# Kernel optimization log

Hardware: AMD Instinct MI355X
Metric: run time of the kernel (lower is better)

The kernel has to match this reference:

```python
import jax, jax.numpy as jnp
import numpy as np


def setup_inputs() -> dict:
    key = jax.random.key(0)
    k1, k2, k3 = jax.random.split(key, 3)
    B, A, CI, CO, E = 2048, 128, 128, 128, 4
    x = jax.random.normal(k1, (B, A, CI), dtype=jnp.float32)
    atom_numbers = jax.random.randint(k2, (B, A), 0, 9, dtype=jnp.int32)
    # glorot-uniform-ish init for W; zeros for b (matches model_ops.zeros)
    limit = np.sqrt(6.0 / (CI + CO)).astype(np.float32)
    W = jax.random.uniform(k3, (E, CI, CO), dtype=jnp.float32, minval=-limit, maxval=limit)
    b = jnp.zeros((E, CO), dtype=jnp.float32)
    atom_cases = jnp.array([1, 6, 7, 8], dtype=jnp.int32)
    return {"x": x, "atom_numbers": atom_numbers, "W": W, "b": b, "atom_cases": atom_cases}


def reference(x, atom_numbers, W, b, atom_cases):
    # Per-expert dense: h[e,b,a,o] = relu(x[b,a,:] @ W[e] + b[e])
    h = jax.nn.relu(jnp.einsum('bai,eio->ebao', x, W) + b[:, None, None, :])
    # mask[e,b,a] = 1 where atom_numbers == atom_cases[e]
    mask = (atom_numbers[None, :, :] == atom_cases[:, None, None]).astype(x.dtype)
    # masked sum over experts -> [B, max_atoms, out_channels]
    return jnp.einsum('ebao,eba->bao', h, mask)
```

## Files before the change

### kernel.cpp

```cpp
#include <hip/hip_runtime.h>
#include <hip/hip_bf16.h>
#include <stdint.h>


typedef __attribute__((ext_vector_type(8))) short short8;
typedef __attribute__((ext_vector_type(4))) float f32x4;

#define PERM_U32_OFF 65536
#define BUCKET_CAP   262144
#define OST_STRIDE   132

union U16 { uint4 u; short8 s; };

__device__ __forceinline__ int bucket_of(int v, int c0, int c1, int c2, int c3) {
    return (v == c0) ? 0 : (v == c1) ? 1 : (v == c2) ? 2 : (v == c3) ? 3 : 4;
}

__device__ __forceinline__ uint32_t pkbf(float lo, float hi) {
    __hip_bfloat162 h = __float22bfloat162_rn(make_float2(lo, hi));
    uint32_t r;
    __builtin_memcpy(&r, &h, 4);
    return r;
}

__global__ __launch_bounds__(256) void k_prep(const float* __restrict__ W,
                                              uint32_t* __restrict__ ws) {
    if (blockIdx.x == 0 && threadIdx.x < 8) ws[threadIdx.x] = 0u;
    const int T   = blockIdx.x * 256 + threadIdx.x;
    const int c16 = T & 15;
    const int g   = (T >> 4) & 3;
    const int nt  = (T >> 6) & 7;
    const int kk  = (T >> 9) & 3;
    const int e   = (T >> 11) & 3;
    float v[8];
    #pragma unroll
    for (int j = 0; j < 8; ++j)
        v[j] = W[(size_t)(e * 128 + kk * 32 + g * 8 + j) * 128 + nt * 16 + c16];
    uint4 pack = make_uint4(pkbf(v[0], v[1]), pkbf(v[2], v[3]),
                            pkbf(v[4], v[5]), pkbf(v[6], v[7]));
    const int lane = g * 16 + c16;
    *(uint4*)((char*)ws + 1024 + e * 32768 + ((kk * 8 + nt) * 64 + lane) * 16) = pack;
}

__global__ __launch_bounds__(256) void k_scatter(const int* __restrict__ an,
                                                 const int* __restrict__ cases,
                                                 uint32_t* __restrict__ ws) {
    __shared__ uint32_t lc[5], lbase[5];
    if (threadIdx.x < 5) lc[threadIdx.x] = 0u;
    __syncthreads();
    const int c0 = cases[0], c1 = cases[1], c2 = cases[2], c3 = cases[3];
    const int r0 = (blockIdx.x * 256 + threadIdx.x) * 4;
    const int4 a = *(const int4*)(an + r0);
    int bk[4];
    bk[0] = bucket_of(a.x, c0, c1, c2, c3);
    bk[1] = bucket_of(a.y, c0, c1, c2, c3);
    bk[2] = bucket_of(a.z, c0, c1, c2, c3);
    bk[3] = bucket_of(a.w, c0, c1, c2, c3);
    uint32_t slot[4];
    #pragma unroll
    for (int i = 0; i < 4; ++i) slot[i] = atomicAdd(&lc[bk[i]], 1u);
    __syncthreads();
    if (threadIdx.x < 5) lbase[threadIdx.x] = atomicAdd(&ws[threadIdx.x], lc[threadIdx.x]);
    __syncthreads();
    uint32_t* __restrict__ perm = ws + PERM_U32_OFF;
    #pragma unroll
    for (int i = 0; i < 4; ++i)
        perm[bk[i] * BUCKET_CAP + lbase[bk[i]] + slot[i]] = (uint32_t)(r0 + i);
}

__global__ __launch_bounds__(512, 4) void k_gemm(const float* __restrict__ x,
                                                 const float* __restrict__ bvec,
                                                 const uint32_t* __restrict__ ws,
                                                 float* __restrict__ out) {
    __shared__ int   ridx[128];
    __shared__ float ost[128 * OST_STRIDE];

    int b = -1, chunk = 0, accb = 0;
    #pragma unroll
    for (int bb = 0; bb < 5; ++bb) {
        const int nb = (int)((ws[bb] + 127u) >> 7);
        if (b < 0 && (int)blockIdx.x < accb + nb) { b = bb; chunk = blockIdx.x - accb; }
        accb += nb;
    }
    if (b < 0) return;

    const int cb   = (int)ws[b];
    const int rbeg = chunk << 7;
    const int nval = min(128, cb - rbeg);
    const uint32_t* __restrict__ perm = ws + PERM_U32_OFF + (size_t)b * BUCKET_CAP;
    if (threadIdx.x < 128)
        ridx[threadIdx.x] = (threadIdx.x < nval) ? (int)perm[rbeg + threadIdx.x] : -1;
    __syncthreads();

    const int lane = threadIdx.x & 63;
    const int wv   = threadIdx.x >> 6;

    if (b == 4) {
        const int half = lane >> 5, l32 = lane & 31;
        const float4 z = make_float4(0.f, 0.f, 0.f, 0.f);
        #pragma unroll
        for (int it = 0; it < 8; ++it) {
            const int r = ridx[wv * 16 + it * 2 + half];
            if (r >= 0) *(float4*)(out + (size_t)r * 128 + l32 * 4) = z;
        }
        return;
    }

    const int g4  = lane >> 4;
    const int c16 = lane & 15;
    const int rg  = wv >> 2;
    const int ng  = wv & 3;

    const float bv0 = bvec[b * 128 + (ng * 2 + 0) * 16 + c16];
    const float bv1 = bvec[b * 128 + (ng * 2 + 1) * 16 + c16];

    int arow[4];
    #pragma unroll
    for (int mf = 0; mf < 4; ++mf) arow[mf] = ridx[rg * 64 + mf * 16 + c16];

    f32x4 acc[4][2];
    #pragma unroll
    for (int mf = 0; mf < 4; ++mf) {
        acc[mf][0] = (f32x4){0.f, 0.f, 0.f, 0.f};
        acc[mf][1] = (f32x4){0.f, 0.f, 0.f, 0.f};
    }

    const uint4* __restrict__ wf = (const uint4*)((const char*)ws + 1024 + b * 32768);

    #pragma unroll
    for (int kk = 0; kk < 4; ++kk) {
        U16 wb0, wb1;
        wb0.u = wf[(kk * 8 + ng * 2 + 0) * 64 + lane];
        wb1.u = wf[(kk * 8 + ng * 2 + 1) * 64 + lane];
        short8 afr[4];
        #pragma unroll
        for (int mf = 0; mf < 4; ++mf) {
            float4 fa = make_float4(0.f, 0.f, 0.f, 0.f);
            float4 fb = make_float4(0.f, 0.f, 0.f, 0.f);
            if (arow[mf] >= 0) {
                const float* p = x + (size_t)arow[mf] * 128 + kk * 32 + g4 * 8;
                fa = *(const float4*)p;
                fb = *(const float4*)(p + 4);
            }
            U16 av;
            av.u = make_uint4(pkbf(fa.x, fa.y), pkbf(fa.z, fa.w),
                              pkbf(fb.x, fb.y), pkbf(fb.z, fb.w));
            afr[mf] = av.s;
        }
        #pragma unroll
        for (int mf = 0; mf < 4; ++mf) {
            acc[mf][0] = __builtin_amdgcn_mfma_f32_16x16x32_bf16(afr[mf], wb0.s, acc[mf][0], 0, 0, 0);
            acc[mf][1] = __builtin_amdgcn_mfma_f32_16x16x32_bf16(afr[mf], wb1.s, acc[mf][1], 0, 0, 0);
        }
    }

    #pragma unroll
    for (int mf = 0; mf < 4; ++mf) {
        #pragma unroll
        for (int r = 0; r < 4; ++r) {
            const int row = rg * 64 + mf * 16 + g4 * 4 + r;
            ost[row * OST_STRIDE + (ng * 2 + 0) * 16 + c16] = fmaxf(acc[mf][0][r] + bv0, 0.f);
            ost[row * OST_STRIDE + (ng * 2 + 1) * 16 + c16] = fmaxf(acc[mf][1][r] + bv1, 0.f);
        }
    }
    __syncthreads();

    const int l32 = lane & 31, lh = lane >> 5;
    #pragma unroll
    for (int i = 0; i < 8; ++i) {
        const int row  = wv * 16 + i * 2 + lh;
        const int orow = ridx[row];
        if (orow >= 0) {
            const float4 vv = *(const float4*)&ost[row * OST_STRIDE + l32 * 4];
            *(float4*)(out + (size_t)orow * 128 + l32 * 4) = vv;
        }
    }
}

extern "C" void kernel_launch(void* const* d_in, const int* in_sizes, int n_in,
                              void* d_out, int out_size, void* d_ws, size_t ws_size,
                              hipStream_t stream) {
    const float* x     = (const float*)d_in[0];
    const int*   an    = (const int*)d_in[1];
    const float* W     = (const float*)d_in[2];
    const float* bvec  = (const float*)d_in[3];
    const int*   cases = (const int*)d_in[4];
    float*    out = (float*)d_out;
    uint32_t* ws  = (uint32_t*)d_ws;

    k_prep   <<<32,   256, 0, stream>>>(W, ws);
    k_scatter<<<256,  256, 0, stream>>>(an, cases, ws);
    k_gemm   <<<2052, 512, 0, stream>>>(x, bvec, ws, out);
}
```

Baseline: 242.7 us.

## Fuse global scatter and GEMM into per-block local bucketing kernel

Removes the separate global scatter kernel and its atomics and permutation buffer. Each block of 256 rows now buckets its rows by expert in shared memory and processes 16-row units per wave, each covering all 128 output columns. This drops one launch and the global perm round-trip, and gives more coalesced locality. The cost is partial 16-row tiles per expert per block, which wastes MFMA work, and each wave reloads the full weight tile for every unit.

Result: no change. 243.5 us (+0.3%).

```diff
diff --git a/kernel.cpp b/kernel.cpp
--- a/kernel.cpp
+++ b/kernel.cpp
@@ -6,26 +6,17 @@
 typedef __attribute__((ext_vector_type(8))) short short8;
 typedef __attribute__((ext_vector_type(4))) float f32x4;
 
-#define PERM_U32_OFF 65536
-#define BUCKET_CAP   262144
-#define OST_STRIDE   132
+#define PSTRIDE 132
 
 union U16 { uint4 u; short8 s; };
 
-__device__ __forceinline__ int bucket_of(int v, int c0, int c1, int c2, int c3) {
-    return (v == c0) ? 0 : (v == c1) ? 1 : (v == c2) ? 2 : (v == c3) ? 3 : 4;
-}
-
 __device__ __forceinline__ uint32_t pkbf(float lo, float hi) {
     __hip_bfloat162 h = __float22bfloat162_rn(make_float2(lo, hi));
-    uint32_t r;
-    __builtin_memcpy(&r, &h, 4);
-    return r;
+    uint32_t r; __builtin_memcpy(&r, &h, 4); return r;
 }
 
 __global__ __launch_bounds__(256) void k_prep(const float* __restrict__ W,
                                               uint32_t* __restrict__ ws) {
-    if (blockIdx.x == 0 && threadIdx.x < 8) ws[threadIdx.x] = 0u;
     const int T   = blockIdx.x * 256 + threadIdx.x;
     const int c16 = T & 15;
     const int g   = (T >> 4) & 3;
@@ -38,141 +29,120 @@
         v[j] = W[(size_t)(e * 128 + kk * 32 + g * 8 + j) * 128 + nt * 16 + c16];
     uint4 pack = make_uint4(pkbf(v[0], v[1]), pkbf(v[2], v[3]),
                             pkbf(v[4], v[5]), pkbf(v[6], v[7]));
-    const int lane = g * 16 + c16;
-    *(uint4*)((char*)ws + 1024 + e * 32768 + ((kk * 8 + nt) * 64 + lane) * 16) = pack;
+    *(uint4*)((char*)ws + 1024 + e * 32768 + ((kk * 8 + nt) * 64 + (g * 16 + c16)) * 16) = pack;
 }
 
-__global__ __launch_bounds__(256) void k_scatter(const int* __restrict__ an,
-                                                 const int* __restrict__ cases,
-                                                 uint32_t* __restrict__ ws) {
-    __shared__ uint32_t lc[5], lbase[5];
-    if (threadIdx.x < 5) lc[threadIdx.x] = 0u;
-    __syncthreads();
-    const int c0 = cases[0], c1 = cases[1], c2 = cases[2], c3 = cases[3];
-    const int r0 = (blockIdx.x * 256 + threadIdx.x) * 4;
-    const int4 a = *(const int4*)(an + r0);
-    int bk[4];
-    bk[0] = bucket_of(a.x, c0, c1, c2, c3);
-    bk[1] = bucket_of(a.y, c0, c1, c2, c3);
-    bk[2] = bucket_of(a.z, c0, c1, c2, c3);
-    bk[3] = bucket_of(a.w, c0, c1, c2, c3);
-    uint32_t slot[4];
-    #pragma unroll
-    for (int i = 0; i < 4; ++i) slot[i] = atomicAdd(&lc[bk[i]], 1u);
-    __syncthreads();
-    if (threadIdx.x < 5) lbase[threadIdx.x] = atomicAdd(&ws[threadIdx.x], lc[threadIdx.x]);
-    __syncthreads();
-    uint32_t* __restrict__ perm = ws + PERM_U32_OFF;
-    #pragma unroll
-    for (int i = 0; i < 4; ++i)
-        perm[bk[i] * BUCKET_CAP + lbase[bk[i]] + slot[i]] = (uint32_t)(r0 + i);
-}
+__global__ __launch_bounds__(256, 4) void k_fused(const float* __restrict__ x,
+                                                  const int*   __restrict__ an,
+                                                  const float* __restrict__ bvec,
+                                                  const int*   __restrict__ cases,
+                                                  const uint32_t* __restrict__ ws,
+                                                  float* __restrict__ out) {
+    __shared__ uint32_t cnt[5], curs[5], start[5];
+    __shared__ uint8_t  units[24];
+    __shared__ int      nunits_s;
+    __shared__ uint16_t lridx[256];
+    __shared__ float    patch[4][16 * PSTRIDE];
 
-__global__ __launch_bounds__(512, 4) void k_gemm(const float* __restrict__ x,
-                                                 const float* __restrict__ bvec,
-                                                 const uint32_t* __restrict__ ws,
-                                                 float* __restrict__ out) {
-    __shared__ int   ridx[128];
-    __shared__ float ost[128 * OST_STRIDE];
+    const int tid  = threadIdx.x;
+    const int lane = tid & 63, wv = tid >> 6;
+    const int r0   = blockIdx.x << 8;
 
-    int b = -1, chunk = 0, accb = 0;
-    #pragma unroll
-    for (int bb = 0; bb < 5; ++bb) {
-        const int nb = (int)((ws[bb] + 127u) >> 7);
-        if (b < 0 && (int)blockIdx.x < accb + nb) { b = bb; chunk = blockIdx.x - accb; }
-        accb += nb;
-    }
-    if (b < 0) return;
-
-    const int cb   = (int)ws[b];
-    const int rbeg = chunk << 7;
-    const int nval = min(128, cb - rbeg);
-    const uint32_t* __restrict__ perm = ws + PERM_U32_OFF + (size_t)b * BUCKET_CAP;
-    if (threadIdx.x < 128)
-        ridx[threadIdx.x] = (threadIdx.x < nval) ? (int)perm[rbeg + threadIdx.x] : -1;
+    if (tid < 5) cnt[tid] = 0;
     __syncthreads();
 
-    const int lane = threadIdx.x & 63;
-    const int wv   = threadIdx.x >> 6;
+    const int c0 = cases[0], c1 = cases[1], c2 = cases[2], c3 = cases[3];
+    const int a  = an[r0 + tid];
+    const int bk = (a == c0) ? 0 : (a == c1) ? 1 : (a == c2) ? 2 : (a == c3) ? 3 : 4;
+    atomicAdd(&cnt[bk], 1u);
+    __syncthreads();
 
-    if (b == 4) {
-        const int half = lane >> 5, l32 = lane & 31;
-        const float4 z = make_float4(0.f, 0.f, 0.f, 0.f);
+    if (tid == 0) {
+        int n = 0; uint32_t run = 0;
         #pragma unroll
-        for (int it = 0; it < 8; ++it) {
-            const int r = ridx[wv * 16 + it * 2 + half];
-            if (r >= 0) *(float4*)(out + (size_t)r * 128 + l32 * 4) = z;
+        for (int b = 0; b < 5; ++b) {
+            start[b] = run; curs[b] = run;
+            const int m = ((int)cnt[b] + 15) >> 4;
+            for (int g = 0; g < m; ++g) units[n++] = (uint8_t)((b << 5) | g);
+            run += cnt[b];
         }
-        return;
+        nunits_s = n;
     }
+    __syncthreads();
 
-    const int g4  = lane >> 4;
-    const int c16 = lane & 15;
-    const int rg  = wv >> 2;
-    const int ng  = wv & 3;
+    const uint32_t slot = atomicAdd(&curs[bk], 1u);
+    lridx[slot] = (uint16_t)tid;
+    __syncthreads();
 
-    const float bv0 = bvec[b * 128 + (ng * 2 + 0) * 16 + c16];
-    const float bv1 = bvec[b * 128 + (ng * 2 + 1) * 16 + c16];
+    const int nunits = nunits_s;
+    const int c16 = lane & 15, g4 = lane >> 4;
+    const int sl8 = lane & 7,  r8 = lane >> 3;
 
-    int arow[4];
-    #pragma unroll
-    for (int mf = 0; mf < 4; ++mf) arow[mf] = ridx[rg * 64 + mf * 16 + c16];
+    for (int ui = wv; ui < nunits; ui += 4) {
+        const int ub   = units[ui] >> 5, ug = units[ui] & 31;
+        const int sb   = (int)start[ub];
+        const int nb   = (int)cnt[ub];
 
-    f32x4 acc[4][2];
-    #pragma unroll
-    for (int mf = 0; mf < 4; ++mf) {
-        acc[mf][0] = (f32x4){0.f, 0.f, 0.f, 0.f};
-        acc[mf][1] = (f32x4){0.f, 0.f, 0.f, 0.f};
-    }
+        if (ub == 4) {
+            const float4 z = make_float4(0.f, 0.f, 0.f, 0.f);
+            #pragma unroll
+            for (int h = 0; h < 2; ++h) {
+                const int rr = r8 + h * 8;
+                if (ug * 16 + rr < nb) {
+                    float* op = out + (size_t)(r0 + lridx[sb + ug * 16 + rr]) * 128 + sl8 * 4;
+                    #pragma unroll
+                    for (int q = 0; q < 4; ++q) *(float4*)(op + q * 32) = z;
+                }
+            }
+            continue;
+        }
 
-    const uint4* __restrict__ wf = (const uint4*)((const char*)ws + 1024 + b * 32768);
+        const int rloc = ug * 16 + c16;
+        const int arow = (rloc < nb) ? (r0 + (int)lridx[sb + rloc]) : -1;
 
-    #pragma unroll
-    for (int kk = 0; kk < 4; ++kk) {
-        U16 wb0, wb1;
-        wb0.u = wf[(kk * 8 + ng * 2 + 0) * 64 + lane];
-        wb1.u = wf[(kk * 8 + ng * 2 + 1) * 64 + lane];
-        short8 afr[4];
+        f32x4 acc[8];
         #pragma unroll
-        for (int mf = 0; mf < 4; ++mf) {
+        for (int n = 0; n < 8; ++n) acc[n] = (f32x4){0.f, 0.f, 0.f, 0.f};
+
+        const uint4* __restrict__ wf = (const uint4*)((const char*)ws + 1024 + ub * 32768);
+
+        #pragma unroll
+        for (int kk = 0; kk < 4; ++kk) {
             float4 fa = make_float4(0.f, 0.f, 0.f, 0.f);
             float4 fb = make_float4(0.f, 0.f, 0.f, 0.f);
-            if (arow[mf] >= 0) {
-                const float* p = x + (size_t)arow[mf] * 128 + kk * 32 + g4 * 8;
+            if (arow >= 0) {
+                const float* p = x + (size_t)arow * 128 + kk * 32 + g4 * 8;
                 fa = *(const float4*)p;
                 fb = *(const float4*)(p + 4);
             }
             U16 av;
             av.u = make_uint4(pkbf(fa.x, fa.y), pkbf(fa.z, fa.w),
                               pkbf(fb.x, fb.y), pkbf(fb.z, fb.w));
-            afr[mf] = av.s;
+            #pragma unroll
+            for (int nt = 0; nt < 8; ++nt) {
+                U16 wb; wb.u = wf[(kk * 8 + nt) * 64 + lane];
+                acc[nt] = __builtin_amdgcn_mfma_f32_16x16x32_bf16(av.s, wb.s, acc[nt], 0, 0, 0);
+            }
         }
+
+        float* pt = &patch[wv][0];
         #pragma unroll
-        for (int mf = 0; mf < 4; ++mf) {
-            acc[mf][0] = __builtin_amdgcn_mfma_f32_16x16x32_bf16(afr[mf], wb0.s, acc[mf][0], 0, 0, 0);
-            acc[mf][1] = __builtin_amdgcn_mfma_f32_16x16x32_bf16(afr[mf], wb1.s, acc[mf][1], 0, 0, 0);
+        for (int nt = 0; nt < 8; ++nt) {
+            const float bb = bvec[ub * 128 + nt * 16 + c16];
+            #pragma unroll
+            for (int r = 0; r < 4; ++r)
+                pt[(g4 * 4 + r) * PSTRIDE + nt * 16 + c16] = fmaxf(acc[nt][r] + bb, 0.f);
         }
-    }
 
-    #pragma unroll
-    for (int mf = 0; mf < 4; ++mf) {
         #pragma unroll
-        for (int r = 0; r < 4; ++r) {
-            const int row = rg * 64 + mf * 16 + g4 * 4 + r;
-            ost[row * OST_STRIDE + (ng * 2 + 0) * 16 + c16] = fmaxf(acc[mf][0][r] + bv0, 0.f);
-            ost[row * OST_STRIDE + (ng * 2 + 1) * 16 + c16] = fmaxf(acc[mf][1][r] + bv1, 0.f);
-        }
-    }
-    __syncthreads();
-
-    const int l32 = lane & 31, lh = lane >> 5;
-    #pragma unroll
-    for (int i = 0; i < 8; ++i) {
-        const int row  = wv * 16 + i * 2 + lh;
-        const int orow = ridx[row];
-        if (orow >= 0) {
-            const float4 vv = *(const float4*)&ost[row * OST_STRIDE + l32 * 4];
-            *(float4*)(out + (size_t)orow * 128 + l32 * 4) = vv;
+        for (int h = 0; h < 2; ++h) {
+            const int rr = r8 + h * 8;
+            if (ug * 16 + rr < nb) {
+                float* op = out + (size_t)(r0 + lridx[sb + ug * 16 + rr]) * 128 + sl8 * 4;
+                #pragma unroll
+                for (int q = 0; q < 4; ++q)
+                    *(float4*)(op + q * 32) = *(const float4*)&pt[rr * PSTRIDE + q * 32 + sl8 * 4];
+            }
         }
     }
 }
@@ -188,7 +158,6 @@
     float*    out = (float*)d_out;
     uint32_t* ws  = (uint32_t*)d_ws;
 
-    k_prep   <<<32,   256, 0, stream>>>(W, ws);
-    k_scatter<<<256,  256, 0, stream>>>(an, cases, ws);
-    k_gemm   <<<2052, 512, 0, stream>>>(x, bvec, ws, out);
+    k_prep <<<32,   256, 0, stream>>>(W, ws);
+    k_fused<<<1024, 256, 0, stream>>>(x, an, bvec, cases, ws, out);
 }
```
